# Performance work log

Measured on AMD Instinct MI355X. Metric: run time of the kernel, lower is better.

Reference implementation:

```python
import jax, jax.numpy as jnp
import numpy as np


def _bit_reversal_perm(N, num_stages):
    idx = np.arange(N)
    perm = np.zeros(N, dtype=np.int64)
    for _ in range(num_stages):
        perm = (perm << 1) | (idx & 1)
        idx >>= 1
    return perm


def setup_inputs() -> dict:
    key = jax.random.key(0)
    k1, k2 = jax.random.split(key)
    B, N = 4096, 4096
    return {
        "x_re": jax.random.normal(k1, (B, N), dtype=jnp.float32),
        "x_im": jax.random.normal(k2, (B, N), dtype=jnp.float32),
    }


def reference(x_re, x_im):
    # Radix-2 DIT FFT, identical math to HollywoodFFT.forward.
    N = x_re.shape[-1]
    num_stages = int(round(np.log2(N)))
    batch = x_re.shape[:-1]

    # Input permutation is pure wiring: bit-reversal gather.
    perm = jnp.asarray(_bit_reversal_perm(N, num_stages))
    y_re = x_re[..., perm]
    y_im = x_im[..., perm]

    # Twiddle tile: W_N^k = exp(-2*pi*i*k/N) (precomputed constants).
    k = np.arange(N)
    ang = -2.0 * np.pi * k / N
    W_re_all = np.cos(ang).astype(np.float32)
    W_im_all = np.sin(ang).astype(np.float32)

    for s in range(num_stages):  # fixed small loop over log2(N) stages
        stride = 1 << s
        group_size = stride << 1
        # twiddle_idx = j * (N // group_size) for j in [0, stride), same for every group
        tw = np.arange(stride) * (N // group_size)
        W_re = jnp.asarray(W_re_all[tw])  # (stride,)
        W_im = jnp.asarray(W_im_all[tw])

        # (..., N) -> (..., N//group_size, 2, stride): [...,g,0,j]=upper, [...,g,1,j]=lower
        yr = y_re.reshape(*batch, N // group_size, 2, stride)
        yi = y_im.reshape(*batch, N // group_size, 2, stride)
        a_re, b_re = yr[..., 0, :], yr[..., 1, :]
        a_im, b_im = yi[..., 0, :], yi[..., 1, :]

        wb_re = W_re * b_re - W_im * b_im
        wb_im = W_re * b_im + W_im * b_re

        y_re = jnp.stack([a_re + wb_re, a_re - wb_re], axis=-2).reshape(*batch, N)
        y_im = jnp.stack([a_im + wb_im, a_im - wb_im], axis=-2).reshape(*batch, N)

    return y_re, y_im
```

## Files before the change

### kernel.cpp

```cpp
#include <hip/hip_runtime.h>


#define NFFT 4096

__device__ __forceinline__ void fft16(float xr[16], float xi[16]) {
    const int br[16] = {0,8,4,12,2,10,6,14,1,9,5,13,3,11,7,15};
    float yr[16], yi[16];
#pragma unroll
    for (int j = 0; j < 16; ++j) { yr[j] = xr[br[j]]; yi[j] = xi[br[j]]; }
    const float W16r[8] = { 1.0f,  0.92387953251128675613f,  0.70710678118654752440f,
                            0.38268343236508977173f,  0.0f, -0.38268343236508977173f,
                           -0.70710678118654752440f, -0.92387953251128675613f };
    const float W16i[8] = { 0.0f, -0.38268343236508977173f, -0.70710678118654752440f,
                           -0.92387953251128675613f, -1.0f, -0.92387953251128675613f,
                           -0.70710678118654752440f, -0.38268343236508977173f };
#pragma unroll
    for (int s = 0; s < 4; ++s) {
        const int stride = 1 << s;
        const int tm = 8 >> s;
#pragma unroll
        for (int g = 0; g < 16; g += 2 * stride) {
#pragma unroll
            for (int p = 0; p < stride; ++p) {
                const int i0 = g + p, i1 = i0 + stride;
                const float twr = W16r[p * tm], twi = W16i[p * tm];
                const float brr = yr[i1] * twr - yi[i1] * twi;
                const float bii = yr[i1] * twi + yi[i1] * twr;
                const float ar = yr[i0], ai = yi[i0];
                yr[i0] = ar + brr; yi[i0] = ai + bii;
                yr[i1] = ar - brr; yi[i1] = ai - bii;
            }
        }
    }
#pragma unroll
    for (int j = 0; j < 16; ++j) { xr[j] = yr[j]; xi[j] = yi[j]; }
}

__global__ __launch_bounds__(256, 5)
void HollywoodFFT_53584011985637_kernel(const float* __restrict__ xre,
                                        const float* __restrict__ xim,
                                        float* __restrict__ outre,
                                        float* __restrict__ outim) {
    __shared__ __align__(16) float2 l[NFFT];

    const int t = threadIdx.x;
    const long long row = blockIdx.x;
    const float* __restrict__ xr_row = xre + row * NFFT;
    const float* __restrict__ xi_row = xim + row * NFFT;

    float vr[16], vi[16];
    const int a = t & 15;
    const int h = t >> 4;

#pragma unroll
    for (int c = 0; c < 16; ++c) {
        vr[c] = xr_row[t + 256 * c];
        vi[c] = xi_row[t + 256 * c];
    }
    fft16(vr, vi);
#pragma unroll
    for (int uu = 0; uu < 16; ++uu) {
        l[a + 16 * (h ^ uu) + 256 * uu] = make_float2(vr[uu], vi[uu]);
    }
    __syncthreads();

    {
        float s0, c0;
        __sincosf(-6.28318530717958647692f * (float)h * (1.0f / 256.0f), &s0, &c0);
        float twr = 1.0f, twi = 0.0f;
#pragma unroll
        for (int bb = 0; bb < 16; ++bb) {
            const float2 xv = l[a + 16 * (bb ^ h) + 256 * h];
            vr[bb] = xv.x * twr - xv.y * twi;
            vi[bb] = xv.x * twi + xv.y * twr;
            const float ntr = twr * c0 - twi * s0;
            twi = twr * s0 + twi * c0;
            twr = ntr;
        }
    }
    fft16(vr, vi);
    __syncthreads();
#pragma unroll
    for (int v = 0; v < 16; ++v) {
        l[(a ^ h) + 16 * (h ^ v) + 256 * v] = make_float2(vr[v], vi[v]);
    }
    __syncthreads();

    const int u2 = a, v2 = h;
    {
        float s0, c0;
        __sincosf(-6.28318530717958647692f * (float)(u2 + 16 * v2) * (1.0f / 4096.0f),
                  &s0, &c0);
        float twr = 1.0f, twi = 0.0f;
#pragma unroll
        for (int aa = 0; aa < 16; ++aa) {
            const float2 xv = l[(aa ^ u2) + 16 * (u2 ^ v2) + 256 * v2];
            vr[aa] = xv.x * twr - xv.y * twi;
            vi[aa] = xv.x * twi + xv.y * twr;
            const float ntr = twr * c0 - twi * s0;
            twi = twr * s0 + twi * c0;
            twr = ntr;
        }
    }
    fft16(vr, vi);

    float* __restrict__ or_row = outre + row * NFFT;
    float* __restrict__ oi_row = outim + row * NFFT;
#pragma unroll
    for (int w = 0; w < 16; ++w) {
        __builtin_nontemporal_store(vr[w], or_row + t + 256 * w);
        __builtin_nontemporal_store(vi[w], oi_row + t + 256 * w);
    }
}

extern "C" void kernel_launch(void* const* d_in, const int* in_sizes, int n_in,
                              void* d_out, int out_size, void* d_ws, size_t ws_size,
                              hipStream_t stream) {
    const float* xre = (const float*)d_in[0];
    const float* xim = (const float*)d_in[1];
    const int B = in_sizes[0] / NFFT;
    float* out = (float*)d_out;
    float* outre = out;
    float* outim = out + (size_t)B * NFFT;
    HollywoodFFT_53584011985637_kernel<<<dim3(B), dim3(256), 0, stream>>>(
        xre, xim, outre, outim);
}
```

Before: 235.8 us.

## Use persistent blocks with software-prefetched next-row loads overlapping FFT compute

Turns the one-block-per-row kernel into a grid-stride persistent kernel with 1024 blocks, each looping over rows. Global loads for the next row are issued into registers while the current row is still being computed, so memory latency overlaps compute. Twiddle sincos values are computed once per block instead of per row. The prefetch buffer adds register pressure, so occupancy is lowered to 4 blocks per SIMD, and an extra barrier is needed before shared memory is reused.

```diff
diff --git a/kernel.cpp b/kernel.cpp
--- a/kernel.cpp
+++ b/kernel.cpp
@@ -36,80 +36,102 @@
     for (int j = 0; j < 16; ++j) { xr[j] = yr[j]; xi[j] = yi[j]; }
 }
 
-__global__ __launch_bounds__(256, 5)
+__global__ __launch_bounds__(256, 4)
 void HollywoodFFT_53584011985637_kernel(const float* __restrict__ xre,
                                         const float* __restrict__ xim,
                                         float* __restrict__ outre,
-                                        float* __restrict__ outim) {
+                                        float* __restrict__ outim,
+                                        int B) {
     __shared__ __align__(16) float2 l[NFFT];
 
     const int t = threadIdx.x;
-    const long long row = blockIdx.x;
-    const float* __restrict__ xr_row = xre + row * NFFT;
-    const float* __restrict__ xi_row = xim + row * NFFT;
-
-    float vr[16], vi[16];
     const int a = t & 15;
     const int h = t >> 4;
 
+    float sB, cB;
+    __sincosf(-6.28318530717958647692f * (float)h * (1.0f / 256.0f), &sB, &cB);
+    float sC, cC;
+    __sincosf(-6.28318530717958647692f * (float)t * (1.0f / 4096.0f), &sC, &cC);
+
+    const int G = gridDim.x;
+    int row = blockIdx.x;
+
+    float pr[16], pi[16];
+    {
+        const float* __restrict__ xr_row = xre + (long long)row * NFFT;
+        const float* __restrict__ xi_row = xim + (long long)row * NFFT;
 #pragma unroll
-    for (int c = 0; c < 16; ++c) {
-        vr[c] = xr_row[t + 256 * c];
-        vi[c] = xi_row[t + 256 * c];
-    }
-    fft16(vr, vi);
-#pragma unroll
-    for (int uu = 0; uu < 16; ++uu) {
-        l[a + 16 * (h ^ uu) + 256 * uu] = make_float2(vr[uu], vi[uu]);
-    }
-    __syncthreads();
-
-    {
-        float s0, c0;
-        __sincosf(-6.28318530717958647692f * (float)h * (1.0f / 256.0f), &s0, &c0);
-        float twr = 1.0f, twi = 0.0f;
-#pragma unroll
-        for (int bb = 0; bb < 16; ++bb) {
-            const float2 xv = l[a + 16 * (bb ^ h) + 256 * h];
-            vr[bb] = xv.x * twr - xv.y * twi;
-            vi[bb] = xv.x * twi + xv.y * twr;
-            const float ntr = twr * c0 - twi * s0;
-            twi = twr * s0 + twi * c0;
-            twr = ntr;
+        for (int c = 0; c < 16; ++c) {
+            pr[c] = xr_row[t + 256 * c];
+            pi[c] = xi_row[t + 256 * c];
         }
     }
-    fft16(vr, vi);
-    __syncthreads();
+
+    while (row < B) {
+        const int next = row + G;
+
+        fft16(pr, pi);
 #pragma unroll
-    for (int v = 0; v < 16; ++v) {
-        l[(a ^ h) + 16 * (h ^ v) + 256 * v] = make_float2(vr[v], vi[v]);
-    }
-    __syncthreads();
+        for (int uu = 0; uu < 16; ++uu) {
+            l[a + 16 * (h ^ uu) + 256 * uu] = make_float2(pr[uu], pi[uu]);
+        }
 
-    const int u2 = a, v2 = h;
-    {
-        float s0, c0;
-        __sincosf(-6.28318530717958647692f * (float)(u2 + 16 * v2) * (1.0f / 4096.0f),
-                  &s0, &c0);
-        float twr = 1.0f, twi = 0.0f;
+        if (next < B) {
+            const float* __restrict__ xr_row = xre + (long long)next * NFFT;
+            const float* __restrict__ xi_row = xim + (long long)next * NFFT;
 #pragma unroll
-        for (int aa = 0; aa < 16; ++aa) {
-            const float2 xv = l[(aa ^ u2) + 16 * (u2 ^ v2) + 256 * v2];
-            vr[aa] = xv.x * twr - xv.y * twi;
-            vi[aa] = xv.x * twi + xv.y * twr;
-            const float ntr = twr * c0 - twi * s0;
-            twi = twr * s0 + twi * c0;
-            twr = ntr;
+            for (int c = 0; c < 16; ++c) {
+                pr[c] = xr_row[t + 256 * c];
+                pi[c] = xi_row[t + 256 * c];
+            }
         }
-    }
-    fft16(vr, vi);
+        __syncthreads();
 
-    float* __restrict__ or_row = outre + row * NFFT;
-    float* __restrict__ oi_row = outim + row * NFFT;
+        float vr[16], vi[16];
+        {
+            float twr = 1.0f, twi = 0.0f;
 #pragma unroll
-    for (int w = 0; w < 16; ++w) {
-        __builtin_nontemporal_store(vr[w], or_row + t + 256 * w);
-        __builtin_nontemporal_store(vi[w], oi_row + t + 256 * w);
+            for (int bb = 0; bb < 16; ++bb) {
+                const float2 xv = l[a + 16 * (bb ^ h) + 256 * h];
+                vr[bb] = xv.x * twr - xv.y * twi;
+                vi[bb] = xv.x * twi + xv.y * twr;
+                const float ntr = twr * cB - twi * sB;
+                twi = twr * sB + twi * cB;
+                twr = ntr;
+            }
+        }
+        fft16(vr, vi);
+        __syncthreads();
+#pragma unroll
+        for (int v = 0; v < 16; ++v) {
+            l[(a ^ h) + 16 * (h ^ v) + 256 * v] = make_float2(vr[v], vi[v]);
+        }
+        __syncthreads();
+
+        {
+            float twr = 1.0f, twi = 0.0f;
+#pragma unroll
+            for (int aa = 0; aa < 16; ++aa) {
+                const float2 xv = l[(aa ^ a) + 16 * (a ^ h) + 256 * h];
+                vr[aa] = xv.x * twr - xv.y * twi;
+                vi[aa] = xv.x * twi + xv.y * twr;
+                const float ntr = twr * cC - twi * sC;
+                twi = twr * sC + twi * cC;
+                twr = ntr;
+            }
+        }
+        __syncthreads();
+        fft16(vr, vi);
+
+        float* __restrict__ or_row = outre + (long long)row * NFFT;
+        float* __restrict__ oi_row = outim + (long long)row * NFFT;
+#pragma unroll
+        for (int w = 0; w < 16; ++w) {
+            __builtin_nontemporal_store(vr[w], or_row + t + 256 * w);
+            __builtin_nontemporal_store(vi[w], oi_row + t + 256 * w);
+        }
+
+        row = next;
     }
 }
 
@@ -122,6 +144,7 @@
     float* out = (float*)d_out;
     float* outre = out;
     float* outim = out + (size_t)B * NFFT;
-    HollywoodFFT_53584011985637_kernel<<<dim3(B), dim3(256), 0, stream>>>(
-        xre, xim, outre, outim);
+    const int G = (B >= 1024) ? 1024 : B;
+    HollywoodFFT_53584011985637_kernel<<<dim3(G), dim3(256), 0, stream>>>(
+        xre, xim, outre, outim, B);
 }
```

Result: slower. 305.3 us (+29.5%).
